# Kernel tuning notes

Hardware: AMD Instinct MI355X
Metric: run time of the kernel (lower is better)

Reference implementation:

```python
import jax, jax.numpy as jnp
import numpy as np


def setup_inputs() -> dict:
    key = jax.random.key(0)
    ks = jax.random.split(key, 6)
    m, d, n, p = 4096, 1024, 16, 1024  # tokens, input_dim, num_experts, output_dim (=slots)
    h = (d + p) * 2 // 3  # 1365, hidden_dim per original module
    s = 0.02
    return {
        "x": jax.random.normal(ks[0], (m, d), jnp.float32),
        "phi": jax.random.normal(ks[1], (d, n, p), jnp.float32) * s,
        "W1": jax.random.normal(ks[2], (n, d, h), jnp.float32) * s,
        "b1": jax.random.normal(ks[3], (n, h), jnp.float32) * s,
        "W2": jax.random.normal(ks[4], (n, h, p), jnp.float32) * s,
        "b2": jax.random.normal(ks[5], (n, p), jnp.float32) * s,
    }


def reference(x, phi, W1, b1, W2, b2):
    # logits: [m, n, p] = tokens x experts x slots
    logits = jnp.einsum('md,dnp->mnp', x, phi)
    # Dispatch weights: softmax over tokens' expert axis (dim=1 in torch == experts n)
    D = jax.nn.softmax(logits, axis=1)
    # Combine weights: softmax over all (expert, slot) pairs per token
    m = logits.shape[0]
    C = jax.nn.softmax(logits.reshape(m, -1), axis=-1).reshape(logits.shape)
    # Slot inputs: [n, p, d]
    Xs = jnp.einsum('md,mnp->npd', x, D)
    # Batched per-expert MLP (replaces the Python loop over experts)
    H = jax.nn.relu(jnp.einsum('npd,ndh->nph', Xs, W1) + b1[:, None, :])
    Ys = jnp.einsum('nph,nho->npo', H, W2) + b2[:, None, :]  # [n, p, out]
    # Combine: [m, out]; flatten(start_dim=1) on a 2D tensor is a no-op
    Y = jnp.einsum('npo,mnp->mo', Ys, C)
    return Y
```

## Files before the change

kernel.cpp:

```cpp
#include <hip/hip_runtime.h>
#include <math.h>

#define MTOK 4096
#define DDIM 1024
#define NEXP 16
#define PSLOT 1024
#define NPDIM 16384
#define HDIM 1365
#define HPAD 1376
#define KSPL 4

typedef unsigned short u16;
typedef __attribute__((ext_vector_type(8))) short short8;
typedef __attribute__((ext_vector_type(8))) unsigned short ushort8;
typedef __attribute__((ext_vector_type(4))) float f32x4;

template<bool Bc, typename T, typename F> struct cond_t { using type = T; };
template<typename T, typename F> struct cond_t<false, T, F> { using type = F; };

__device__ __forceinline__ float b2f(u16 v) {
    union { unsigned int u; float f; } x;
    x.u = ((unsigned int)v) << 16;
    return x.f;
}
__device__ __forceinline__ u16 f2b(float f) {
    union { float f; unsigned int u; } x;
    x.f = f;
    unsigned int r = x.u + 0x7FFFu + ((x.u >> 16) & 1u);
    return (u16)(r >> 16);
}
__device__ __forceinline__ void stv(float* p, long long i, float v) { p[i] = v; }
__device__ __forceinline__ void stv(u16*  p, long long i, float v) { p[i] = f2b(v); }

template<int AMODE, typename TA, typename TB, typename TC,
         bool BIASF, bool RELUF, bool ROWSC, bool BCHK>
__global__ __launch_bounds__(256) void mgemm(
    const TA* __restrict__ A, long long sA, int lda,
    const TB* __restrict__ B, long long sB, int ldb,
    TC* __restrict__ C, long long sC, int ldc,
    const float* __restrict__ S,
    const float* __restrict__ bias, long long sBias,
    const float* __restrict__ rowsc,
    int M, int N, int NZ, int K, int Kb, int Nb)
{
    constexpr int AS = (AMODE == 0) ? 32 : 40;
    constexpr int BS = 40;
    __shared__ u16 As[2][128 * AS];
    __shared__ u16 Bs[2][128 * BS];

    const int bz = blockIdx.z;
    A += (long long)bz * sA;
    B += (long long)bz * sB;
    C += (long long)bz * sC;
    const float* biasp = BIASF ? (bias + (long long)bz * sBias) : nullptr;

    const int gx = gridDim.x;
    const int nwg = gx * gridDim.y;
    int wg = blockIdx.x + gx * blockIdx.y;
    wg = (wg & 7) * (nwg >> 3) + (wg >> 3);
    const int m0 = (wg / gx) * 128;
    const int n0 = (wg % gx) * 128;

    const int tid  = threadIdx.x;
    const int lane = tid & 63;
    const int wv   = tid >> 6;
    const int wm   = wv & 1;
    const int wn   = wv >> 1;
    const int quad = lane >> 4;
    const int l16  = lane & 15;

    const int pp   = tid & 63;
    const int cl0  = 2 * pp;
    const int ng0  = n0 + cl0;

    f32x4 acc[4][4];
#pragma unroll
    for (int i = 0; i < 4; ++i)
#pragma unroll
        for (int j = 0; j < 4; ++j) acc[i][j] = (f32x4){0.f, 0.f, 0.f, 0.f};

    using BRAW = typename cond_t<sizeof(TB) == 2, unsigned int[8], float[16]>::type;

    auto LOADA = [&](int k0, int buf, unsigned int (&araw)[8]) {
        if constexpr (AMODE == 0) {
#pragma unroll
            for (int q = 0; q < 2; ++q) {
                const u16* gp = A + (long long)(m0 + wv * 32 + q * 16 + (lane >> 2)) * lda
                                  + k0 + (lane & 3) * 8;
                u16* lp = &As[buf][(wv * 32 + q * 16) * 32];
                __builtin_amdgcn_global_load_lds(
                    (const __attribute__((address_space(1))) unsigned int*)gp,
                    (__attribute__((address_space(3))) unsigned int*)lp, 16, 0, 0);
            }
        } else {
#pragma unroll
            for (int i = 0; i < 8; ++i) {
                const long long kg = k0 + wv * 8 + i;
                araw[i] = *(const unsigned int*)((const u16*)A + kg * lda + (m0 + cl0));
            }
        }
    };
    auto WRITEA = [&](int k0, int buf, unsigned int (&araw)[8]) {
        if constexpr (AMODE != 0) {
            ushort8 va, vb;
#pragma unroll
            for (int i = 0; i < 8; ++i) {
                const long long kg = k0 + wv * 8 + i;
                const float2 s = *(const float2*)&S[kg * 1024 + ((m0 + cl0) & 1023)];
                va[i] = f2b(b2f((u16)(araw[i] & 0xFFFFu)) * s.x);
                vb[i] = f2b(b2f((u16)(araw[i] >> 16)) * s.y);
            }
            *(ushort8*)&As[buf][cl0 * AS + wv * 8]       = va;
            *(ushort8*)&As[buf][(cl0 + 1) * AS + wv * 8] = vb;
        }
    };
    auto LOADB = [&](int k0, BRAW& braw) {
        if constexpr (sizeof(TB) == 2) {
#pragma unroll
            for (int i = 0; i < 8; ++i) {
                const int kg = k0 + wv * 8 + i;
                braw[i] = *(const unsigned int*)((const u16*)B + (long long)kg * ldb + ng0);
            }
        } else {
            bool full = true;
            if constexpr (BCHK) full = (k0 + 32 <= Kb) && (n0 + 128 <= Nb);
            if (full) {
#pragma unroll
                for (int i = 0; i < 8; ++i) {
                    const int kg = k0 + wv * 8 + i;
                    const float* bp = (const float*)B + (long long)kg * ldb + ng0;
                    braw[2 * i]     = bp[0];
                    braw[2 * i + 1] = bp[1];
                }
            } else {
#pragma unroll
                for (int i = 0; i < 8; ++i) {
                    const int kg = k0 + wv * 8 + i;
                    float v0 = 0.f, v1 = 0.f;
                    if (kg < Kb) {
                        if (ng0 < Nb)     v0 = ((const float*)B)[(long long)kg * ldb + ng0];
                        if (ng0 + 1 < Nb) v1 = ((const float*)B)[(long long)kg * ldb + ng0 + 1];
                    }
                    braw[2 * i]     = v0;
                    braw[2 * i + 1] = v1;
                }
            }
        }
    };
    auto WRITEB = [&](int buf, BRAW& braw) {
        ushort8 va, vb;
        if constexpr (sizeof(TB) == 2) {
#pragma unroll
            for (int i = 0; i < 8; ++i) {
                va[i] = (u16)(braw[i] & 0xFFFFu);
                vb[i] = (u16)(braw[i] >> 16);
            }
        } else {
#pragma unroll
            for (int i = 0; i < 8; ++i) {
                va[i] = f2b(braw[2 * i]);
                vb[i] = f2b(braw[2 * i + 1]);
            }
        }
        *(ushort8*)&Bs[buf][cl0 * BS + wv * 8]       = va;
        *(ushort8*)&Bs[buf][(cl0 + 1) * BS + wv * 8] = vb;
    };
    auto MM = [&](int buf) {
        short8 bfr[4];
#pragma unroll
        for (int ni = 0; ni < 4; ++ni)
            bfr[ni] = *(const short8*)&Bs[buf][(wn * 64 + ni * 16 + l16) * BS + quad * 8];
#pragma unroll
        for (int mi = 0; mi < 4; ++mi) {
            short8 a = *(const short8*)&As[buf][(wm * 64 + mi * 16 + l16) * AS + quad * 8];
#pragma unroll
            for (int ni = 0; ni < 4; ++ni)
                acc[mi][ni] = __builtin_amdgcn_mfma_f32_16x16x32_bf16(a, bfr[ni], acc[mi][ni], 0, 0, 0);
        }
    };

    const int nt = K >> 5;
    {
        unsigned int araw[8];
        BRAW braw;
        LOADA(0, 0, araw);
        LOADB(0, braw);
        WRITEA(0, 0, araw);
        WRITEB(0, braw);
        __syncthreads();
    }
    for (int t = 0; t < nt; ++t) {
        const int cur = t & 1, nxt = cur ^ 1;
        unsigned int araw[8];
        BRAW braw;
        const bool pf = (t + 1 < nt);
        if (pf) {
            LOADA((t + 1) * 32, nxt, araw);
            LOADB((t + 1) * 32, braw);
        }
        MM(cur);
        if (pf) {
            WRITEA((t + 1) * 32, nxt, araw);
            WRITEB(nxt, braw);
        }
        __syncthreads();
    }

#pragma unroll
    for (int mi = 0; mi < 4; ++mi) {
#pragma unroll
        for (int r = 0; r < 4; ++r) {
            const int rg = m0 + wm * 64 + mi * 16 + quad * 4 + r;
            if (rg >= M) continue;
            const float rs = ROWSC ? rowsc[rg] : 1.f;
#pragma unroll
            for (int ni = 0; ni < 4; ++ni) {
                const int cg = n0 + wn * 64 + ni * 16 + l16;
                if (cg < N) {
                    float v = acc[mi][ni][r];
                    if (BIASF) v += biasp[cg];
                    if (RELUF) v = fmaxf(v, 0.f);
                    if (ROWSC) v *= rs;
                    stv(C, (long long)rg * ldc + cg, v);
                } else if (cg < NZ) {
                    stv(C, (long long)rg * ldc + cg, 0.f);
                }
            }
        }
    }
}

__global__ __launch_bounds__(256) void cvt_k(
    const float* __restrict__ src, u16* __restrict__ dst, long long n)
{
    const long long i = ((long long)blockIdx.x * 256 + threadIdx.x) * 8;
    if (i >= n) return;
    const float4 a = *(const float4*)&src[i];
    const float4 b = *(const float4*)&src[i + 4];
    ushort8 v;
    v[0] = f2b(a.x); v[1] = f2b(a.y); v[2] = f2b(a.z); v[3] = f2b(a.w);
    v[4] = f2b(b.x); v[5] = f2b(b.y); v[6] = f2b(b.z); v[7] = f2b(b.w);
    *(ushort8*)&dst[i] = v;
}

__global__ __launch_bounds__(256) void softmax_k(
    u16* __restrict__ L, float* __restrict__ rsd, float* __restrict__ rsc)
{
    const int m = blockIdx.x;
    u16* row = L + (long long)m * NPDIM;
    const int tid = threadIdx.x;
    __shared__ float red[256];

    float mx = -1e30f;
    for (int i = tid * 8; i < NPDIM; i += 2048) {
        const ushort8 v = *(const ushort8*)&row[i];
#pragma unroll
        for (int j = 0; j < 8; ++j) mx = fmaxf(mx, b2f(v[j]));
    }
    red[tid] = mx;
    __syncthreads();
    for (int s = 128; s > 0; s >>= 1) {
        if (tid < s) red[tid] = fmaxf(red[tid], red[tid + s]);
        __syncthreads();
    }
    const float mxAll = red[0];
    __syncthreads();

    float sum = 0.f;
    for (int i = tid * 8; i < NPDIM; i += 2048) {
        const ushort8 v = *(const ushort8*)&row[i];
        ushort8 e;
#pragma unroll
        for (int j = 0; j < 8; ++j) {
            const float ef = __expf(b2f(v[j]) - mxAll);
            const u16 eb = f2b(ef);
            e[j] = eb;
            sum += b2f(eb);
        }
        *(ushort8*)&row[i] = e;
    }
    red[tid] = sum;
    __syncthreads();
    for (int s = 128; s > 0; s >>= 1) {
        if (tid < s) red[tid] += red[tid + s];
        __syncthreads();
    }
    if (tid == 0) rsc[m] = 1.f / red[0];
    __syncthreads();

    {
        const int p0 = tid * 4;
        float s0 = 0.f, s1 = 0.f, s2 = 0.f, s3 = 0.f;
#pragma unroll
        for (int n = 0; n < NEXP; ++n) {
            const ushort4 v = *(const ushort4*)&row[n * PSLOT + p0];
            s0 += b2f(v.x); s1 += b2f(v.y); s2 += b2f(v.z); s3 += b2f(v.w);
        }
        const float4 r = {1.f / s0, 1.f / s1, 1.f / s2, 1.f / s3};
        *(float4*)&rsd[(long long)m * PSLOT + p0] = r;
    }
}

__global__ __launch_bounds__(256) void reduce_k(
    const float* __restrict__ Yp, float* __restrict__ Y)
{
    const long long S = (long long)MTOK * PSLOT;
    const long long i = ((long long)blockIdx.x * 256 + threadIdx.x) * 4;
    f32x4 r = *(const f32x4*)&Yp[i];
#pragma unroll
    for (int z = 1; z < KSPL; ++z) r += *(const f32x4*)&Yp[(long long)z * S + i];
    *(f32x4*)&Y[i] = r;
}

extern "C" void kernel_launch(void* const* d_in, const int* in_sizes, int n_in,
                              void* d_out, int out_size, void* d_ws, size_t ws_size,
                              hipStream_t stream)
{
    const float* x   = (const float*)d_in[0];
    const float* phi = (const float*)d_in[1];
    const float* W1  = (const float*)d_in[2];
    const float* b1  = (const float*)d_in[3];
    const float* W2  = (const float*)d_in[4];
    const float* b2  = (const float*)d_in[5];
    float* Y = (float*)d_out;

    char* w = (char*)d_ws;
    u16*   L    = (u16*)w;   w += (size_t)MTOK * NPDIM * 2;
    u16*   Ys   = (u16*)w;   w += (size_t)NEXP * PSLOT * PSLOT * 2;
    float* rsc  = (float*)w; w += (size_t)MTOK * 4;
    float* Yp   = (float*)w;
    float* rsd  = (float*)w; w += (size_t)MTOK * PSLOT * 4;
    u16*   Xs   = (u16*)w;   w += (size_t)NEXP * PSLOT * DDIM * 2;
    u16*   Hb   = (u16*)w;   w += (size_t)NEXP * PSLOT * HPAD * 2;
    u16*   phib = Ys;
    u16*   xb   = Hb;

    cvt_k<<<dim3((MTOK * DDIM) / (8 * 256)), 256, 0, stream>>>(x, xb, (long long)MTOK * DDIM);
    cvt_k<<<dim3((DDIM * NPDIM) / (8 * 256)), 256, 0, stream>>>(phi, phib, (long long)DDIM * NPDIM);

    mgemm<0, u16, u16, u16, false, false, false, false>
        <<<dim3(NPDIM / 128, MTOK / 128, 1), 256, 0, stream>>>(
        xb, 0, DDIM,  phib, 0, NPDIM,  L, 0, NPDIM,
        nullptr, nullptr, 0, nullptr,
        MTOK, NPDIM, NPDIM, DDIM, DDIM, NPDIM);

    softmax_k<<<dim3(MTOK), 256, 0, stream>>>(L, rsd, rsc);

    mgemm<2, u16, u16, u16, false, false, false, false>
        <<<dim3(DDIM / 128, NPDIM / 128, 1), 256, 0, stream>>>(
        L, 0, NPDIM,  xb, 0, DDIM,  Xs, 0, DDIM,
        rsd, nullptr, 0, nullptr,
        NPDIM, DDIM, DDIM, MTOK, MTOK, DDIM);

    mgemm<0, u16, float, u16, true, true, false, true>
        <<<dim3((HPAD + 127) / 128, PSLOT / 128, NEXP), 256, 0, stream>>>(
        Xs, (long long)PSLOT * DDIM, DDIM,
        W1, (long long)DDIM * HDIM, HDIM,
        Hb, (long long)PSLOT * HPAD, HPAD,
        nullptr, b1, HDIM, nullptr,
        PSLOT, HDIM, HPAD, DDIM, DDIM, HDIM);

    mgemm<0, u16, float, u16, true, false, false, true>
        <<<dim3(PSLOT / 128, PSLOT / 128, NEXP), 256, 0, stream>>>(
        Hb, (long long)PSLOT * HPAD, HPAD,
        W2, (long long)HDIM * PSLOT, PSLOT,
        Ys, (long long)PSLOT * PSLOT, PSLOT,
        nullptr, b2, PSLOT, nullptr,
        PSLOT, PSLOT, PSLOT, HPAD, HDIM, PSLOT);

    mgemm<0, u16, u16, float, false, false, true, false>
        <<<dim3(PSLOT / 128, MTOK / 128, KSPL), 256, 0, stream>>>(
        L, (long long)(NPDIM / KSPL), NPDIM,
        Ys, (long long)(NPDIM / KSPL) * PSLOT, PSLOT,
        Yp, (long long)MTOK * PSLOT, PSLOT,
        nullptr, nullptr, 0, rsc,
        MTOK, PSLOT, PSLOT, NPDIM / KSPL, NPDIM / KSPL, PSLOT);

    reduce_k<<<dim3((MTOK * PSLOT) / (4 * 256)), 256, 0, stream>>>(Yp, Y);
}
```

Before: 1.374 ms.

## Swizzle GEMM LDS tiles, use hardware bf16 pack conversion, prefetch scale loads

Applies an XOR swizzle to the LDS offsets of the transposed A tile and the B tile, so the per-row 16-byte writes and the MFMA fragment reads hit fewer bank conflicts. The software round-to-nearest bf16 conversion is replaced with the packed v_cvt_pk_bf16_f32 instruction in the GEMM and in the conversion kernel, and the bf16 shuffles are done as 32-bit packed word operations. The dispatch-scale loads are moved from the write phase into the prefetch phase so they overlap with the MFMA work. This costs some extra registers for the staged scales, and the inline asm depends on the instruction being available on this target.

After: 1.347 ms. No clear change (-1.9%).

```diff
diff --git a/kernel.cpp b/kernel.cpp
--- a/kernel.cpp
+++ b/kernel.cpp
@@ -13,6 +13,7 @@
 typedef unsigned short u16;
 typedef __attribute__((ext_vector_type(8))) short short8;
 typedef __attribute__((ext_vector_type(8))) unsigned short ushort8;
+typedef __attribute__((ext_vector_type(4))) unsigned int uint32x4;
 typedef __attribute__((ext_vector_type(4))) float f32x4;
 
 template<bool Bc, typename T, typename F> struct cond_t { using type = T; };
@@ -28,6 +29,11 @@
     x.f = f;
     unsigned int r = x.u + 0x7FFFu + ((x.u >> 16) & 1u);
     return (u16)(r >> 16);
+}
+__device__ __forceinline__ unsigned int cvtpk(float lo, float hi) {
+    unsigned int r;
+    asm("v_cvt_pk_bf16_f32 %0, %1, %2" : "=v"(r) : "v"(lo), "v"(hi));
+    return r;
 }
 __device__ __forceinline__ void stv(float* p, long long i, float v) { p[i] = v; }
 __device__ __forceinline__ void stv(u16*  p, long long i, float v) { p[i] = f2b(v); }
@@ -73,6 +79,15 @@
     const int cl0  = 2 * pp;
     const int ng0  = n0 + cl0;
 
+    auto aoff = [&](int row, int k8) {
+        int o = row * AS + k8 * 8;
+        if constexpr (AMODE != 0) o ^= ((row >> 3) & 3) << 3;
+        return o;
+    };
+    auto boff = [&](int row, int k8) {
+        return (row * BS + k8 * 8) ^ (((row >> 3) & 3) << 3);
+    };
+
     f32x4 acc[4][4];
 #pragma unroll
     for (int i = 0; i < 4; ++i)
@@ -81,7 +96,7 @@
 
     using BRAW = typename cond_t<sizeof(TB) == 2, unsigned int[8], float[16]>::type;
 
-    auto LOADA = [&](int k0, int buf, unsigned int (&araw)[8]) {
+    auto LOADA = [&](int k0, int buf, unsigned int (&araw)[8], float2 (&sr)[8]) {
         if constexpr (AMODE == 0) {
 #pragma unroll
             for (int q = 0; q < 2; ++q) {
@@ -97,21 +112,23 @@
             for (int i = 0; i < 8; ++i) {
                 const long long kg = k0 + wv * 8 + i;
                 araw[i] = *(const unsigned int*)((const u16*)A + kg * lda + (m0 + cl0));
-            }
-        }
-    };
-    auto WRITEA = [&](int k0, int buf, unsigned int (&araw)[8]) {
+                sr[i]   = *(const float2*)&S[kg * 1024 + ((m0 + cl0) & 1023)];
+            }
+        }
+    };
+    auto WRITEA = [&](int buf, unsigned int (&araw)[8], float2 (&sr)[8]) {
         if constexpr (AMODE != 0) {
-            ushort8 va, vb;
-#pragma unroll
-            for (int i = 0; i < 8; ++i) {
-                const long long kg = k0 + wv * 8 + i;
-                const float2 s = *(const float2*)&S[kg * 1024 + ((m0 + cl0) & 1023)];
-                va[i] = f2b(b2f((u16)(araw[i] & 0xFFFFu)) * s.x);
-                vb[i] = f2b(b2f((u16)(araw[i] >> 16)) * s.y);
-            }
-            *(ushort8*)&As[buf][cl0 * AS + wv * 8]       = va;
-            *(ushort8*)&As[buf][(cl0 + 1) * AS + wv * 8] = vb;
+            uint32x4 wa, wb;
+#pragma unroll
+            for (int j = 0; j < 4; ++j) {
+                const unsigned int r0 = araw[2 * j], r1 = araw[2 * j + 1];
+                wa[j] = cvtpk(b2f((u16)(r0 & 0xFFFFu)) * sr[2 * j].x,
+                              b2f((u16)(r1 & 0xFFFFu)) * sr[2 * j + 1].x);
+                wb[j] = cvtpk(b2f((u16)(r0 >> 16)) * sr[2 * j].y,
+                              b2f((u16)(r1 >> 16)) * sr[2 * j + 1].y);
+            }
+            *(uint32x4*)&As[buf][aoff(cl0, wv)]     = wa;
+            *(uint32x4*)&As[buf][aoff(cl0 + 1, wv)] = wb;
         }
     };
     auto LOADB = [&](int k0, BRAW& braw) {
@@ -148,31 +165,32 @@
         }
     };
     auto WRITEB = [&](int buf, BRAW& braw) {
-        ushort8 va, vb;
+        uint32x4 wa, wb;
         if constexpr (sizeof(TB) == 2) {
 #pragma unroll
-            for (int i = 0; i < 8; ++i) {
-                va[i] = (u16)(braw[i] & 0xFFFFu);
-                vb[i] = (u16)(braw[i] >> 16);
+            for (int j = 0; j < 4; ++j) {
+                const unsigned int r0 = braw[2 * j], r1 = braw[2 * j + 1];
+                wa[j] = (r0 & 0xFFFFu) | (r1 << 16);
+                wb[j] = (r0 >> 16) | (r1 & 0xFFFF0000u);
             }
         } else {
 #pragma unroll
-            for (int i = 0; i < 8; ++i) {
-                va[i] = f2b(braw[2 * i]);
-                vb[i] = f2b(braw[2 * i + 1]);
-            }
-        }
-        *(ushort8*)&Bs[buf][cl0 * BS + wv * 8]       = va;
-        *(ushort8*)&Bs[buf][(cl0 + 1) * BS + wv * 8] = vb;
+            for (int j = 0; j < 4; ++j) {
+                wa[j] = cvtpk(braw[4 * j],     braw[4 * j + 2]);
+                wb[j] = cvtpk(braw[4 * j + 1], braw[4 * j + 3]);
+            }
+        }
+        *(uint32x4*)&Bs[buf][boff(cl0, wv)]     = wa;
+        *(uint32x4*)&Bs[buf][boff(cl0 + 1, wv)] = wb;
     };
     auto MM = [&](int buf) {
         short8 bfr[4];
 #pragma unroll
         for (int ni = 0; ni < 4; ++ni)
-            bfr[ni] = *(const short8*)&Bs[buf][(wn * 64 + ni * 16 + l16) * BS + quad * 8];
+            bfr[ni] = *(const short8*)&Bs[buf][boff(wn * 64 + ni * 16 + l16, quad)];
 #pragma unroll
         for (int mi = 0; mi < 4; ++mi) {
-            short8 a = *(const short8*)&As[buf][(wm * 64 + mi * 16 + l16) * AS + quad * 8];
+            short8 a = *(const short8*)&As[buf][aoff(wm * 64 + mi * 16 + l16, quad)];
 #pragma unroll
             for (int ni = 0; ni < 4; ++ni)
                 acc[mi][ni] = __builtin_amdgcn_mfma_f32_16x16x32_bf16(a, bfr[ni], acc[mi][ni], 0, 0, 0);
@@ -182,25 +200,27 @@
     const int nt = K >> 5;
     {
         unsigned int araw[8];
+        float2 sr[8];
         BRAW braw;
-        LOADA(0, 0, araw);
+        LOADA(0, 0, araw, sr);
         LOADB(0, braw);
-        WRITEA(0, 0, araw);
+        WRITEA(0, araw, sr);
         WRITEB(0, braw);
         __syncthreads();
     }
     for (int t = 0; t < nt; ++t) {
         const int cur = t & 1, nxt = cur ^ 1;
         unsigned int araw[8];
+        float2 sr[8];
         BRAW braw;
         const bool pf = (t + 1 < nt);
         if (pf) {
-            LOADA((t + 1) * 32, nxt, araw);
+            LOADA((t + 1) * 32, nxt, araw, sr);
             LOADB((t + 1) * 32, braw);
         }
         MM(cur);
         if (pf) {
-            WRITEA((t + 1) * 32, nxt, araw);
+            WRITEA(nxt, araw, sr);
             WRITEB(nxt, braw);
         }
         __syncthreads();
@@ -237,10 +257,12 @@
     if (i >= n) return;
     const float4 a = *(const float4*)&src[i];
     const float4 b = *(const float4*)&src[i + 4];
-    ushort8 v;
-    v[0] = f2b(a.x); v[1] = f2b(a.y); v[2] = f2b(a.z); v[3] = f2b(a.w);
-    v[4] = f2b(b.x); v[5] = f2b(b.y); v[6] = f2b(b.z); v[7] = f2b(b.w);
-    *(ushort8*)&dst[i] = v;
+    uint32x4 v;
+    v[0] = cvtpk(a.x, a.y);
+    v[1] = cvtpk(a.z, a.w);
+    v[2] = cvtpk(b.x, b.y);
+    v[3] = cvtpk(b.z, b.w);
+    *(uint32x4*)&dst[i] = v;
 }
 
 __global__ __launch_bounds__(256) void softmax_k(
```
